# Kernel tuning notes

Hardware: AMD Instinct MI355X
Metric: run time of the kernel (lower is better)

## Reference

```python
import jax, jax.numpy as jnp
import numpy as np

B, N = 2, 1024
DIM = 1024
DQK = 128
NUM_KEYS = 256
NUM_MEM = NUM_KEYS * NUM_KEYS
TOPK = 32
RANK = 2
HEADS = 2
DV = 512
KCONV = 5
MARGIN = 0.15
AUX_W = 0.1
MEM_LR = 10.0
RMS_EPS = 1.1920929e-07  # torch.finfo(float32).eps (RMSNorm eps=None default)
LN_EPS = 1e-5


def setup_inputs() -> dict:
    key = jax.random.key(0)
    ks = jax.random.split(key, 6)
    return {
        "tokens": jax.random.normal(ks[0], (B, N, DIM), jnp.float32),
        "rms_w": jnp.ones((DIM,), jnp.float32),
        "conv_w": jax.random.normal(ks[1], (DIM, 1, KCONV), jnp.float32) * 0.1,
        "conv_b": jnp.zeros((DIM,), jnp.float32),
        "wq": jax.random.normal(ks[2], (DQK, DIM), jnp.float32) * 0.02,
        "qln_w": jnp.ones((DQK,), jnp.float32),
        "keys": jax.random.normal(ks[3], (2, RANK, NUM_KEYS, DQK), jnp.float32) * 0.01,
        "core": jax.random.normal(ks[4], (HEADS, RANK, RANK), jnp.float32) * 0.01,
        "memories": jax.random.normal(ks[5], (NUM_MEM, DV), jnp.float32) * 0.01,
    }


def _forward(tokens, rms_w, conv_w, conv_b, wq, qln_w, keys, core, memories):
    # prenorm RMSNorm
    x = tokens * jax.lax.rsqrt(jnp.mean(tokens * tokens, -1, keepdims=True) + RMS_EPS) * rms_w
    # SVD of core; rank-1 merge vectors (first left/right singular vectors)
    u, s, vh = jnp.linalg.svd(core, full_matrices=False)
    u_vec = u[..., :, 0]   # (H, R)
    t_vec = vh[..., 0, :]  # (H, R)  == v[..., :, 0]
    aux = jnp.sum(jnp.mean(jnp.square(jax.nn.relu(s[:, 1:] - MARGIN)), -1)) * AUX_W
    # causal depthwise conv (left-pad KCONV-1)
    xc = jnp.swapaxes(x, 1, 2)  # (B, D, N)
    xc = jax.lax.conv_general_dilated(
        xc, conv_w, (1,), [(KCONV - 1, 0)],
        feature_group_count=DIM, dimension_numbers=('NCH', 'OIH', 'NCH'))
    x = jnp.swapaxes(xc + conv_b[None, :, None], 1, 2)
    # queries + LayerNorm (no bias). NOTE: original applies key_ln but then uses
    # the raw self.keys in the einsum, so key normalization is a no-op; replicated.
    q = x @ wq.T
    mu = jnp.mean(q, -1, keepdims=True)
    var = jnp.mean(jnp.square(q - mu), -1, keepdims=True)
    q = (q - mu) * jax.lax.rsqrt(var + LN_EPS) * qln_w
    # product-key scores: (2, B, N, M, R)
    sc = jnp.einsum('bnd,crmd->cbnmr', q, keys)
    row_sc, col_sc = sc[0], sc[1]  # (B, N, M, R)
    m_row = jnp.einsum('bnmr,hr->hbnm', row_sc, u_vec)
    m_col = jnp.einsum('bnmr,hr->hbnm', col_sc, t_vec)
    _, top_row = jax.lax.top_k(m_row, TOPK)  # (H, B, N, K)
    _, top_col = jax.lax.top_k(m_col, TOPK)
    # candidate flat memory indices: outer sum -> (H, B, N, K*K)
    idx = (top_row * NUM_KEYS)[..., :, None] + top_col[..., None, :]
    idx = idx.reshape(HEADS, B, N, TOPK * TOPK)
    # gather per-rank scores at the top row/col keys
    rs = jnp.broadcast_to(row_sc[None], (HEADS,) + row_sc.shape)
    cs = jnp.broadcast_to(col_sc[None], (HEADS,) + col_sc.shape)
    ri = jnp.broadcast_to(top_row[..., None], top_row.shape + (RANK,))
    ci = jnp.broadcast_to(top_col[..., None], top_col.shape + (RANK,))
    f_row = jnp.take_along_axis(rs, ri, axis=3)  # (H, B, N, K, R)
    f_col = jnp.take_along_axis(cs, ci, axis=3)
    # bilinear core combine over ranks -> (H, B, N, K, K)
    scores = jnp.einsum('hbnir,hbnjs,hrs->hbnij', f_row, f_col, core)
    scores = scores.reshape(HEADS, B, N, TOPK * TOPK)
    fs, top_m = jax.lax.top_k(scores, TOPK)
    f_idx = jnp.take_along_axis(idx, top_m, axis=-1)  # (H, B, N, K)
    fs = jax.nn.sigmoid(fs)
    # gather from memory table: (H, B, N, K, DV)
    mem = memories[f_idx]
    # scale_gradient exactly as written: detach(t) - s*t + detach(s*t)  (grad = -s)
    scaled = mem * MEM_LR
    mem = jax.lax.stop_gradient(mem) - scaled + jax.lax.stop_gradient(scaled)
    agg = jnp.einsum('hbnkd,hbnk->hbnd', mem, fs)
    out = jnp.transpose(agg, (1, 2, 0, 3)).reshape(B, N, HEADS * DV)
    # combine_values_to_out is Identity (heads * dim_values == dim)
    return out, aux


def reference(tokens, rms_w, conv_w, conv_b, wq, qln_w, keys, core, memories):
    return _forward(tokens, rms_w, conv_w, conv_b, wq, qln_w, keys, core, memories)
```

## Files before the change

kernel.cpp:

```cpp
#include <hip/hip_runtime.h>
#include <math.h>


#define ROWS 2048
#define RPB 2
#define SLB (RPB + 4)
#define KSPLIT 16

__device__ inline double dsgn(double x, double y) { return (y >= 0.0) ? fabs(x) : -fabs(x); }

__device__ void dlasv2_dev(double f, double g, double h,
                           double& ssmin, double& ssmax,
                           double& snr, double& csr, double& snl, double& csl)
{
  const double EPSD = 2.2204460492503131e-16;
  double ft = f, fa = fabs(f), ht = h, ha = fabs(h);
  int pmax = 1;
  bool swp = (ha > fa);
  if (swp) { pmax = 3; double tp = ft; ft = ht; ht = tp; tp = fa; fa = ha; ha = tp; }
  double gt = g, ga = fabs(gt);
  double clt = 0.0, crt = 0.0, slt = 0.0, srt = 0.0;
  if (ga == 0.0) {
    ssmin = ha; ssmax = fa; clt = 1.0; crt = 1.0; slt = 0.0; srt = 0.0;
  } else {
    bool gasmal = true;
    if (ga > fa) {
      pmax = 2;
      if ((fa / ga) < EPSD) {
        gasmal = false;
        ssmax = ga;
        if (ha > 1.0) ssmin = fa / (ga / ha); else ssmin = (fa / ga) * ha;
        clt = 1.0; slt = ht / gt; srt = 1.0; crt = ft / gt;
      }
    }
    if (gasmal) {
      double dd = fa - ha, l;
      if (dd == fa) l = 1.0; else l = dd / fa;
      double m  = gt / ft;
      double t  = 2.0 - l;
      double mm = m * m, tt = t * t;
      double s  = sqrt(tt + mm);
      double r  = (l == 0.0) ? fabs(m) : sqrt(l * l + mm);
      double a  = 0.5 * (s + r);
      ssmin = ha / a;
      ssmax = fa * a;
      if (mm == 0.0) {
        if (l == 0.0) t = dsgn(2.0, ft) * dsgn(1.0, gt);
        else          t = gt / dsgn(dd, ft) + m / t;
      } else {
        t = (m / (s + t) + m / (r + l)) * (1.0 + a);
      }
      double ll = sqrt(t * t + 4.0);
      crt = 2.0 / ll;
      srt = t / ll;
      clt = (crt + srt * m) / a;
      slt = (ht / ft) * srt / a;
    }
  }
  if (swp) { csl = srt; snl = crt; csr = slt; snr = clt; }
  else     { csl = clt; snl = slt; csr = crt; snr = srt; }
  double tsign = 1.0;
  if (pmax == 1) tsign = dsgn(1.0, csr) * dsgn(1.0, csl) * dsgn(1.0, f);
  if (pmax == 2) tsign = dsgn(1.0, snr) * dsgn(1.0, csl) * dsgn(1.0, g);
  if (pmax == 3) tsign = dsgn(1.0, snr) * dsgn(1.0, snl) * dsgn(1.0, h);
  ssmax = dsgn(ssmax, tsign);
  ssmin = dsgn(ssmin, tsign * dsgn(1.0, f) * dsgn(1.0, h));
}

__device__ void do_svd(const float* __restrict__ core, float* __restrict__ misc,
                       float* __restrict__ aux_out)
{
  double aux = 0.0;
  for (int hh = 0; hh < 2; hh++) {
    double a = (double)core[hh * 4 + 0];
    double b = (double)core[hh * 4 + 1];
    double c = (double)core[hh * 4 + 2];
    double d = (double)core[hh * 4 + 3];
    double tau = 0.0, v2 = 0.0, d1, e, d2;
    if (c != 0.0) {
      double nrm  = sqrt(a * a + c * c);
      double beta = (a >= 0.0) ? -nrm : nrm;
      tau = (beta - a) / beta;
      v2  = c / (a - beta);
      double wsum = b + v2 * d;
      d1 = beta;
      e  = b - tau * wsum;
      d2 = d - tau * v2 * wsum;
    } else { d1 = a; e = b; d2 = d; }
    double ssmin, ssmax, snr, csr, snl, csl;
    dlasv2_dev(d1, e, d2, ssmin, ssmax, snr, csr, snl, csl);
    double t0 = csl + v2 * snl;
    double u0 = csl - tau * t0;
    double u1 = snl - tau * v2 * t0;
    double sg = (ssmax < 0.0) ? -1.0 : 1.0;
    misc[hh * 2 + 0]     = (float)u0;
    misc[hh * 2 + 1]     = (float)u1;
    misc[4 + hh * 2 + 0] = (float)(sg * csr);
    misc[4 + hh * 2 + 1] = (float)(sg * snr);
    double s2 = fabs(ssmin);
    double rl = s2 - 0.15; if (rl < 0.0) rl = 0.0;
    aux += rl * rl;
  }
  aux_out[0] = (float)(aux * 0.1);
}

__global__ __launch_bounds__(256) void conv_kernel(const float* __restrict__ tokens,
                                                   const float* __restrict__ rms_w,
                                                   const float* __restrict__ conv_w,
                                                   const float* __restrict__ conv_b,
                                                   const float* __restrict__ core,
                                                   float* __restrict__ misc,
                                                   float* __restrict__ aux_out,
                                                   float* __restrict__ x2)
{
  __shared__ float x_l[SLB][1024];
  __shared__ float red[SLB][4];
  __shared__ float inv_s[SLB];
  const int t    = threadIdx.x;
  const int row0 = blockIdx.x * RPB;
  const int n0   = row0 & 1023;
  const int c0   = t * 4;

  float sq[SLB];
  #pragma unroll
  for (int s = 0; s < SLB; s++) {
    float4 v = make_float4(0.f, 0.f, 0.f, 0.f);
    if (n0 - 4 + s >= 0)
      v = *(const float4*)(tokens + (size_t)(row0 - 4 + s) * 1024 + c0);
    *(float4*)&x_l[s][c0] = v;
    sq[s] = v.x * v.x + v.y * v.y + v.z * v.z + v.w * v.w;
  }
  #pragma unroll
  for (int off = 32; off; off >>= 1) {
    #pragma unroll
    for (int s = 0; s < SLB; s++) sq[s] += __shfl_down(sq[s], off, 64);
  }
  const int lane = t & 63, wv_id = t >> 6;
  if (lane == 0) {
    #pragma unroll
    for (int s = 0; s < SLB; s++) red[s][wv_id] = sq[s];
  }
  __syncthreads();
  if (t < SLB)
    inv_s[t] = rsqrtf((red[t][0] + red[t][1] + red[t][2] + red[t][3]) * (1.0f / 1024.0f)
                      + 1.1920929e-07f);
  __syncthreads();
  #pragma unroll
  for (int s = 0; s < SLB; s++) {
    float iv = inv_s[s];
    float4 v = *(float4*)&x_l[s][c0];
    v.x *= iv; v.y *= iv; v.z *= iv; v.w *= iv;
    *(float4*)&x_l[s][c0] = v;
  }
  float wv[20];
  const float* cw = conv_w + (size_t)c0 * 5;
  #pragma unroll
  for (int i = 0; i < 5; i++) {
    float4 u = *(const float4*)(cw + i * 4);
    wv[i * 4 + 0] = u.x; wv[i * 4 + 1] = u.y; wv[i * 4 + 2] = u.z; wv[i * 4 + 3] = u.w;
  }
  float4 rw = *(const float4*)(rms_w + c0);
  float4 cb = *(const float4*)(conv_b + c0);
  #pragma unroll
  for (int r = 0; r < RPB; r++) {
    float4 acc = make_float4(0.f, 0.f, 0.f, 0.f);
    #pragma unroll
    for (int k = 0; k < 5; k++) {
      float4 x4 = *(const float4*)&x_l[r + k][c0];
      acc.x = fmaf(x4.x, wv[0 * 5 + k], acc.x);
      acc.y = fmaf(x4.y, wv[1 * 5 + k], acc.y);
      acc.z = fmaf(x4.z, wv[2 * 5 + k], acc.z);
      acc.w = fmaf(x4.w, wv[3 * 5 + k], acc.w);
    }
    acc.x = acc.x * rw.x + cb.x;
    acc.y = acc.y * rw.y + cb.y;
    acc.z = acc.z * rw.z + cb.z;
    acc.w = acc.w * rw.w + cb.w;
    *(float4*)(x2 + (size_t)(row0 + r) * 1024 + c0) = acc;
  }
  if (blockIdx.x == 0 && t == 0) do_svd(core, misc, aux_out);
}

__global__ __launch_bounds__(256) void gemm_kernel(const float* __restrict__ A, int lda,
                                                   const float* __restrict__ Bm, int ldb,
                                                   float* __restrict__ C, int ldc,
                                                   int koffy, int coffy, int poffy)
{
  __shared__ __align__(16) float a_lds[32 * 64];
  __shared__ __align__(16) float b_lds[32 * 128];
  const int t  = threadIdx.x;
  const int rb = blockIdx.x * 64;
  const int kb = blockIdx.y * koffy;
  const int cb = blockIdx.y * coffy;
  C += (size_t)blockIdx.y * (size_t)poffy;
  const int tx = t & 31, ty = t >> 5;
  const int c0 = tx * 4, r0 = ty * 8;
  const int nkt = koffy >> 5;
  float acc[8][4];
  #pragma unroll
  for (int i = 0; i < 8; i++)
    #pragma unroll
    for (int j = 0; j < 4; j++) acc[i][j] = 0.0f;

  const int ra = t & 63,  kqa = (t >> 6) * 8;
  const int ob = t >> 1,  kqb = (t & 1) * 16;

  for (int kt = 0; kt < nkt; kt++) {
    const int k0 = kb + kt * 32;
    {
      const float* ap = A + (size_t)(rb + ra) * lda + k0 + kqa;
      float4 a0 = *(const float4*)(ap);
      float4 a1 = *(const float4*)(ap + 4);
      a_lds[(kqa + 0) * 64 + ra] = a0.x;
      a_lds[(kqa + 1) * 64 + ra] = a0.y;
      a_lds[(kqa + 2) * 64 + ra] = a0.z;
      a_lds[(kqa + 3) * 64 + ra] = a0.w;
      a_lds[(kqa + 4) * 64 + ra] = a1.x;
      a_lds[(kqa + 5) * 64 + ra] = a1.y;
      a_lds[(kqa + 6) * 64 + ra] = a1.z;
      a_lds[(kqa + 7) * 64 + ra] = a1.w;
    }
    {
      const float* bp = Bm + (size_t)(cb + ob) * ldb + k0 + kqb;
      float4 b0 = *(const float4*)(bp);
      float4 b1 = *(const float4*)(bp + 4);
      float4 b2 = *(const float4*)(bp + 8);
      float4 b3 = *(const float4*)(bp + 12);
      b_lds[(kqb +  0) * 128 + ob] = b0.x;
      b_lds[(kqb +  1) * 128 + ob] = b0.y;
      b_lds[(kqb +  2) * 128 + ob] = b0.z;
      b_lds[(kqb +  3) * 128 + ob] = b0.w;
      b_lds[(kqb +  4) * 128 + ob] = b1.x;
      b_lds[(kqb +  5) * 128 + ob] = b1.y;
      b_lds[(kqb +  6) * 128 + ob] = b1.z;
      b_lds[(kqb +  7) * 128 + ob] = b1.w;
      b_lds[(kqb +  8) * 128 + ob] = b2.x;
      b_lds[(kqb +  9) * 128 + ob] = b2.y;
      b_lds[(kqb + 10) * 128 + ob] = b2.z;
      b_lds[(kqb + 11) * 128 + ob] = b2.w;
      b_lds[(kqb + 12) * 128 + ob] = b3.x;
      b_lds[(kqb + 13) * 128 + ob] = b3.y;
      b_lds[(kqb + 14) * 128 + ob] = b3.z;
      b_lds[(kqb + 15) * 128 + ob] = b3.w;
    }
    __syncthreads();
    #pragma unroll
    for (int k = 0; k < 32; k++) {
      float4 av0 = *(const float4*)(a_lds + k * 64 + r0);
      float4 av1 = *(const float4*)(a_lds + k * 64 + r0 + 4);
      float4 bv  = *(const float4*)(b_lds + k * 128 + c0);
      float ar[8] = {av0.x, av0.y, av0.z, av0.w, av1.x, av1.y, av1.z, av1.w};
      float br[4] = {bv.x, bv.y, bv.z, bv.w};
      #pragma unroll
      for (int i = 0; i < 8; i++)
        #pragma unroll
        for (int j = 0; j < 4; j++)
          acc[i][j] = fmaf(ar[i], br[j], acc[i][j]);
    }
    __syncthreads();
  }
  #pragma unroll
  for (int i = 0; i < 8; i++) {
    float4 o4; o4.x = acc[i][0]; o4.y = acc[i][1]; o4.z = acc[i][2]; o4.w = acc[i][3];
    *(float4*)(C + (size_t)(rb + r0 + i) * ldc + cb + c0) = o4;
  }
}

__global__ __launch_bounds__(256) void gemm2ln_kernel(const float* __restrict__ qpart,
                                                      const float* __restrict__ qln_w,
                                                      const float* __restrict__ keys,
                                                      float* __restrict__ C)
{
  __shared__ __align__(16) float a_l[128 * 32];
  __shared__ __align__(16) float b_lds[32 * 128];
  const int t  = threadIdx.x;
  const int rb = blockIdx.x * 32;
  const int cb = blockIdx.y * 128;

  const int l32 = t & 31;
  const int g32 = t >> 5;
  float vs[4][4];
  #pragma unroll
  for (int j = 0; j < 4; j++) { vs[j][0]=0.f; vs[j][1]=0.f; vs[j][2]=0.f; vs[j][3]=0.f; }
  #pragma unroll
  for (int g = 0; g < KSPLIT; g++) {
    const float* pg = qpart + (size_t)g * (ROWS * 128) + (size_t)rb * 128 + l32 * 4;
    #pragma unroll
    for (int j = 0; j < 4; j++) {
      float4 v = *(const float4*)(pg + (g32 + 8 * j) * 128);
      vs[j][0] += v.x; vs[j][1] += v.y; vs[j][2] += v.z; vs[j][3] += v.w;
    }
  }
  float4 qw = *(const float4*)(qln_w + l32 * 4);
  #pragma unroll
  for (int j = 0; j < 4; j++) {
    float s1 = vs[j][0] + vs[j][1] + vs[j][2] + vs[j][3];
    #pragma unroll
    for (int off = 16; off; off >>= 1) s1 += __shfl_xor(s1, off, 32);
    float mu = s1 * (1.0f / 128.0f);
    float d0 = vs[j][0] - mu, d1 = vs[j][1] - mu, d2 = vs[j][2] - mu, d3 = vs[j][3] - mu;
    float s2 = d0 * d0 + d1 * d1 + d2 * d2 + d3 * d3;
    #pragma unroll
    for (int off = 16; off; off >>= 1) s2 += __shfl_xor(s2, off, 32);
    float rstd = rsqrtf(s2 * (1.0f / 128.0f) + 1e-5f);
    const int row = g32 + 8 * j;
    a_l[(l32 * 4 + 0) * 32 + row] = d0 * rstd * qw.x;
    a_l[(l32 * 4 + 1) * 32 + row] = d1 * rstd * qw.y;
    a_l[(l32 * 4 + 2) * 32 + row] = d2 * rstd * qw.z;
    a_l[(l32 * 4 + 3) * 32 + row] = d3 * rstd * qw.w;
  }
  __syncthreads();

  const int tx = t & 31, ty = t >> 5;
  const int c0 = tx * 4, r0 = ty * 4;
  float acc[4][4];
  #pragma unroll
  for (int i = 0; i < 4; i++)
    #pragma unroll
    for (int j = 0; j < 4; j++) acc[i][j] = 0.0f;

  const int ob = t >> 1, kqb = (t & 1) * 16;
  for (int kt = 0; kt < 4; kt++) {
    const int k0 = kt * 32;
    {
      const float* bp = keys + (size_t)(cb + ob) * 128 + k0 + kqb;
      float4 b0 = *(const float4*)(bp);
      float4 b1 = *(const float4*)(bp + 4);
      float4 b2 = *(const float4*)(bp + 8);
      float4 b3 = *(const float4*)(bp + 12);
      b_lds[(kqb +  0) * 128 + ob] = b0.x;
      b_lds[(kqb +  1) * 128 + ob] = b0.y;
      b_lds[(kqb +  2) * 128 + ob] = b0.z;
      b_lds[(kqb +  3) * 128 + ob] = b0.w;
      b_lds[(kqb +  4) * 128 + ob] = b1.x;
      b_lds[(kqb +  5) * 128 + ob] = b1.y;
      b_lds[(kqb +  6) * 128 + ob] = b1.z;
      b_lds[(kqb +  7) * 128 + ob] = b1.w;
      b_lds[(kqb +  8) * 128 + ob] = b2.x;
      b_lds[(kqb +  9) * 128 + ob] = b2.y;
      b_lds[(kqb + 10) * 128 + ob] = b2.z;
      b_lds[(kqb + 11) * 128 + ob] = b2.w;
      b_lds[(kqb + 12) * 128 + ob] = b3.x;
      b_lds[(kqb + 13) * 128 + ob] = b3.y;
      b_lds[(kqb + 14) * 128 + ob] = b3.z;
      b_lds[(kqb + 15) * 128 + ob] = b3.w;
    }
    __syncthreads();
    #pragma unroll
    for (int k = 0; k < 32; k++) {
      float4 av = *(const float4*)(a_l + (k0 + k) * 32 + r0);
      float4 bv = *(const float4*)(b_lds + k * 128 + c0);
      float ar[4] = {av.x, av.y, av.z, av.w};
      float br[4] = {bv.x, bv.y, bv.z, bv.w};
      #pragma unroll
      for (int i = 0; i < 4; i++)
        #pragma unroll
        for (int j = 0; j < 4; j++)
          acc[i][j] = fmaf(ar[i], br[j], acc[i][j]);
    }
    __syncthreads();
  }
  #pragma unroll
  for (int i = 0; i < 4; i++) {
    float4 o4; o4.x = acc[i][0]; o4.y = acc[i][1]; o4.z = acc[i][2]; o4.w = acc[i][3];
    *(float4*)(C + (size_t)(rb + r0 + i) * 1024 + cb + c0) = o4;
  }
}

__device__ inline unsigned f2ord(float f) {
  unsigned u = __float_as_uint(f);
  return (u & 0x80000000u) ? ~u : (u | 0x80000000u);
}
__device__ inline int lpc(unsigned long long m) {
  return __builtin_amdgcn_mbcnt_hi((unsigned)(m >> 32),
         __builtin_amdgcn_mbcnt_lo((unsigned)m, 0));
}

__global__ __launch_bounds__(256) void tail_kernel(const float* __restrict__ sc,
                                                   const float* __restrict__ misc,
                                                   const float* __restrict__ core,
                                                   const float* __restrict__ memories,
                                                   float* __restrict__ out)
{
  __shared__ __align__(16) float s_pl[1024];
  __shared__ int   tkbuf[4][32];
  __shared__ float mvals[4][32];
  __shared__ int   mcand[4][32];
  __shared__ int   s_idx[64];
  __shared__ float s_w[64];

  const int row = blockIdx.x;
  const int tid = threadIdx.x;
  ((float4*)s_pl)[tid] = ((const float4*)(sc + (size_t)row * 1024))[tid];
  __syncthreads();

  const int w = tid >> 6, lane = tid & 63;

  {
    const int h = w >> 1, side = w & 1;
    const float v0 = misc[side * 4 + h * 2 + 0];
    const float v1 = misc[side * 4 + h * 2 + 1];
    const float* p0 = s_pl + side * 512;
    const float* p1 = p0 + 256;
    const int mb = lane * 4;
    float4 a4 = *(const float4*)(p0 + mb);
    float4 b4 = *(const float4*)(p1 + mb);
    unsigned kk[4];
    kk[0] = f2ord(a4.x * v0 + b4.x * v1);
    kk[1] = f2ord(a4.y * v0 + b4.y * v1);
    kk[2] = f2ord(a4.z * v0 + b4.z * v1);
    kk[3] = f2ord(a4.w * v0 + b4.w * v1);
    unsigned tau = 0u;
    #pragma unroll
    for (int b = 31; b >= 0; --b) {
      unsigned cand = tau | (1u << b);
      int cnt = 0;
      #pragma unroll
      for (int i = 0; i < 4; i++) cnt += __popcll(__ballot(kk[i] >= cand));
      if (cnt >= 32) tau = cand;
    }
    unsigned long long bG[4], bE[4];
    int cntG = 0, sbG = 0, sbE = 0;
    #pragma unroll
    for (int i = 0; i < 4; i++) {
      bG[i] = __ballot(kk[i] > tau);
      bE[i] = __ballot(kk[i] == tau);
      cntG += __popcll(bG[i]);
      sbG  += lpc(bG[i]);
      sbE  += lpc(bE[i]);
    }
    const int need = 32 - cntG;
    int runG = 0, runE = 0;
    #pragma unroll
    for (int i = 0; i < 4; i++) {
      if (kk[i] > tau)       { tkbuf[w][sbG + runG] = mb + i; runG++; }
      else if (kk[i] == tau) {
        int r = sbE + runE;
        if (r < need) tkbuf[w][cntG + r] = mb + i;
        runE++;
      }
    }
  }
  __syncthreads();

  {
    const int h = w >> 1, half = w & 1;
    const float c00 = core[h * 4 + 0], c01 = core[h * 4 + 1];
    const float c10 = core[h * 4 + 2], c11 = core[h * 4 + 3];
    const int i_glob = half * 16 + (lane >> 2);
    const int ri = tkbuf[h * 2 + 0][i_glob];
    const float fr0 = s_pl[ri], fr1 = s_pl[256 + ri];
    const float a0 = fr0 * c00 + fr1 * c10;
    const float a1 = fr0 * c01 + fr1 * c11;
    const int j0 = (lane & 3) * 8;
    float sv[8];
    unsigned kk[8];
    #pragma unroll
    for (int t2 = 0; t2 < 8; t2++) {
      int cj = tkbuf[h * 2 + 1][j0 + t2];
      sv[t2] = a0 * s_pl[512 + cj] + a1 * s_pl[768 + cj];
      kk[t2] = f2ord(sv[t2]);
    }
    unsigned tau = 0u;
    #pragma unroll
    for (int b = 31; b >= 0; --b) {
      unsigned cand = tau | (1u << b);
      int cnt = 0;
      #pragma unroll
      for (int i = 0; i < 8; i++) cnt += __popcll(__ballot(kk[i] >= cand));
      if (cnt >= 32) tau = cand;
    }
    unsigned long long bG[8], bE[8];
    int cntG = 0, sbG = 0, sbE = 0;
    #pragma unroll
    for (int i = 0; i < 8; i++) {
      bG[i] = __ballot(kk[i] > tau);
      bE[i] = __ballot(kk[i] == tau);
      cntG += __popcll(bG[i]);
      sbG  += lpc(bG[i]);
      sbE  += lpc(bE[i]);
    }
    const int need = 32 - cntG;
    int runG = 0, runE = 0;
    #pragma unroll
    for (int i = 0; i < 8; i++) {
      int c = i_glob * 32 + j0 + i;
      if (kk[i] > tau) {
        mvals[w][sbG + runG] = sv[i]; mcand[w][sbG + runG] = c; runG++;
      } else if (kk[i] == tau) {
        int r = sbE + runE;
        if (r < need) { mvals[w][cntG + r] = sv[i]; mcand[w][cntG + r] = c; }
        runE++;
      }
    }
  }
  __syncthreads();

  if (w < 2) {
    const int h = w;
    const int half2 = lane >> 5, k = lane & 31;
    const float v = mvals[h * 2 + half2][k];
    const int   c = mcand[h * 2 + half2][k];
    int cnt = 0;
    #pragma unroll 8
    for (int j = 0; j < 64; j++) {
      float u = mvals[h * 2 + (j >> 5)][j & 31];
      int  uc = mcand[h * 2 + (j >> 5)][j & 31];
      cnt += (u > v || (u == v && uc < c)) ? 1 : 0;
    }
    if (cnt < 32) {
      int ii = c >> 5, jj = c & 31;
      s_idx[h * 32 + cnt] = tkbuf[h * 2][ii] * 256 + tkbuf[h * 2 + 1][jj];
      s_w[h * 32 + cnt]   = 1.0f / (1.0f + expf(-v));
    }
  }
  __syncthreads();

  const int h2 = tid >> 7;
  const int d4 = tid & 127;
  const int base = h2 * 32;
  const float* mb = memories + d4 * 4;
  float ax = 0.f, ay = 0.f, az = 0.f, aw = 0.f;
  float4 va[8], vb[8];
  float  wa[8], wb[8];
  #pragma unroll
  for (int i = 0; i < 8; i++) {
    int mi = s_idx[base + i]; wa[i] = s_w[base + i];
    va[i] = *(const float4*)(mb + (size_t)mi * 512);
  }
  #pragma unroll
  for (int i = 0; i < 8; i++) {
    int mi = s_idx[base + 8 + i]; wb[i] = s_w[base + 8 + i];
    vb[i] = *(const float4*)(mb + (size_t)mi * 512);
  }
  #pragma unroll
  for (int i = 0; i < 8; i++) {
    ax = fmaf(wa[i], va[i].x, ax); ay = fmaf(wa[i], va[i].y, ay);
    az = fmaf(wa[i], va[i].z, az); aw = fmaf(wa[i], va[i].w, aw);
  }
  #pragma unroll
  for (int i = 0; i < 8; i++) {
    int mi = s_idx[base + 16 + i]; wa[i] = s_w[base + 16 + i];
    va[i] = *(const float4*)(mb + (size_t)mi * 512);
  }
  #pragma unroll
  for (int i = 0; i < 8; i++) {
    ax = fmaf(wb[i], vb[i].x, ax); ay = fmaf(wb[i], vb[i].y, ay);
    az = fmaf(wb[i], vb[i].z, az); aw = fmaf(wb[i], vb[i].w, aw);
  }
  #pragma unroll
  for (int i = 0; i < 8; i++) {
    int mi = s_idx[base + 24 + i]; wb[i] = s_w[base + 24 + i];
    vb[i] = *(const float4*)(mb + (size_t)mi * 512);
  }
  #pragma unroll
  for (int i = 0; i < 8; i++) {
    ax = fmaf(wa[i], va[i].x, ax); ay = fmaf(wa[i], va[i].y, ay);
    az = fmaf(wa[i], va[i].z, az); aw = fmaf(wa[i], va[i].w, aw);
  }
  #pragma unroll
  for (int i = 0; i < 8; i++) {
    ax = fmaf(wb[i], vb[i].x, ax); ay = fmaf(wb[i], vb[i].y, ay);
    az = fmaf(wb[i], vb[i].z, az); aw = fmaf(wb[i], vb[i].w, aw);
  }
  float4 o4; o4.x = ax; o4.y = ay; o4.z = az; o4.w = aw;
  ((float4*)out)[(size_t)row * 256 + tid] = o4;
}

extern "C" void kernel_launch(void* const* d_in, const int* in_sizes, int n_in,
                              void* d_out, int out_size, void* d_ws, size_t ws_size,
                              hipStream_t stream) {
  const float* tokens = (const float*)d_in[0];
  const float* rms_w  = (const float*)d_in[1];
  const float* conv_w = (const float*)d_in[2];
  const float* conv_b = (const float*)d_in[3];
  const float* wq     = (const float*)d_in[4];
  const float* qln_w  = (const float*)d_in[5];
  const float* keys   = (const float*)d_in[6];
  const float* core   = (const float*)d_in[7];
  const float* mems   = (const float*)d_in[8];
  float* out = (float*)d_out;
  float* ws  = (float*)d_ws;

  float* misc   = ws;
  float* x2     = ws + 4096;
  float* qpart  = x2 + 2097152;
  float* sc     = x2;

  conv_kernel  <<<ROWS / RPB, 256, 0, stream>>>(tokens, rms_w, conv_w, conv_b,
                                                core, misc, out + 2097152, x2);
  gemm_kernel  <<<dim3(32, KSPLIT), 256, 0, stream>>>(x2, 1024, wq, 1024,
                                                      qpart, 128, 1024 / KSPLIT, 0,
                                                      ROWS * 128);
  gemm2ln_kernel<<<dim3(64, 8), 256, 0, stream>>>(qpart, qln_w, keys, sc);
  tail_kernel  <<<ROWS, 256, 0, stream>>>(sc, misc, core, mems, out);
}
```

Before: 275.9 us.

## Fuse causal depthwise conv into query GEMM A-tile load, keep only RMS stats

Replaces the conv kernel, which wrote the full convolved activation to workspace, with a small kernel that only computes per-row RMS scale factors plus the SVD. The depthwise conv is now computed on the fly inside the query GEMM while it builds the A tile in shared memory, using a 68-row halo of tokens. This removes an 8 MB write and re-read of the intermediate activation. In exchange the GEMM does redundant conv work and halo loads, the split-K factor drops from 16 to 8, and each block now runs a longer 128-wide K loop with extra syncs.

```diff
diff --git a/kernel.cpp b/kernel.cpp
--- a/kernel.cpp
+++ b/kernel.cpp
@@ -3,9 +3,7 @@
 
 
 #define ROWS 2048
-#define RPB 2
-#define SLB (RPB + 4)
-#define KSPLIT 16
+#define KSPLIT 8
 
 __device__ inline double dsgn(double x, double y) { return (y >= 0.0) ? fabs(x) : -fabs(x); }
 
@@ -104,151 +102,119 @@
   aux_out[0] = (float)(aux * 0.1);
 }
 
-__global__ __launch_bounds__(256) void conv_kernel(const float* __restrict__ tokens,
-                                                   const float* __restrict__ rms_w,
-                                                   const float* __restrict__ conv_w,
-                                                   const float* __restrict__ conv_b,
-                                                   const float* __restrict__ core,
-                                                   float* __restrict__ misc,
-                                                   float* __restrict__ aux_out,
-                                                   float* __restrict__ x2)
+__global__ __launch_bounds__(256) void rms_kernel(const float* __restrict__ tokens,
+                                                  const float* __restrict__ core,
+                                                  float* __restrict__ inv_sg,
+                                                  float* __restrict__ misc,
+                                                  float* __restrict__ aux_out)
 {
-  __shared__ float x_l[SLB][1024];
-  __shared__ float red[SLB][4];
-  __shared__ float inv_s[SLB];
+  __shared__ float red[8][4];
   const int t    = threadIdx.x;
-  const int row0 = blockIdx.x * RPB;
-  const int n0   = row0 & 1023;
+  const int row0 = blockIdx.x * 8;
   const int c0   = t * 4;
-
-  float sq[SLB];
-  #pragma unroll
-  for (int s = 0; s < SLB; s++) {
-    float4 v = make_float4(0.f, 0.f, 0.f, 0.f);
-    if (n0 - 4 + s >= 0)
-      v = *(const float4*)(tokens + (size_t)(row0 - 4 + s) * 1024 + c0);
-    *(float4*)&x_l[s][c0] = v;
+  float sq[8];
+  #pragma unroll
+  for (int s = 0; s < 8; s++) {
+    float4 v = *(const float4*)(tokens + (size_t)(row0 + s) * 1024 + c0);
     sq[s] = v.x * v.x + v.y * v.y + v.z * v.z + v.w * v.w;
   }
   #pragma unroll
   for (int off = 32; off; off >>= 1) {
     #pragma unroll
-    for (int s = 0; s < SLB; s++) sq[s] += __shfl_down(sq[s], off, 64);
-  }
-  const int lane = t & 63, wv_id = t >> 6;
+    for (int s = 0; s < 8; s++) sq[s] += __shfl_down(sq[s], off, 64);
+  }
+  const int lane = t & 63, w = t >> 6;
   if (lane == 0) {
     #pragma unroll
-    for (int s = 0; s < SLB; s++) red[s][wv_id] = sq[s];
+    for (int s = 0; s < 8; s++) red[s][w] = sq[s];
   }
   __syncthreads();
-  if (t < SLB)
-    inv_s[t] = rsqrtf((red[t][0] + red[t][1] + red[t][2] + red[t][3]) * (1.0f / 1024.0f)
-                      + 1.1920929e-07f);
-  __syncthreads();
-  #pragma unroll
-  for (int s = 0; s < SLB; s++) {
-    float iv = inv_s[s];
-    float4 v = *(float4*)&x_l[s][c0];
-    v.x *= iv; v.y *= iv; v.z *= iv; v.w *= iv;
-    *(float4*)&x_l[s][c0] = v;
-  }
-  float wv[20];
-  const float* cw = conv_w + (size_t)c0 * 5;
-  #pragma unroll
-  for (int i = 0; i < 5; i++) {
-    float4 u = *(const float4*)(cw + i * 4);
-    wv[i * 4 + 0] = u.x; wv[i * 4 + 1] = u.y; wv[i * 4 + 2] = u.z; wv[i * 4 + 3] = u.w;
-  }
-  float4 rw = *(const float4*)(rms_w + c0);
-  float4 cb = *(const float4*)(conv_b + c0);
-  #pragma unroll
-  for (int r = 0; r < RPB; r++) {
-    float4 acc = make_float4(0.f, 0.f, 0.f, 0.f);
-    #pragma unroll
-    for (int k = 0; k < 5; k++) {
-      float4 x4 = *(const float4*)&x_l[r + k][c0];
-      acc.x = fmaf(x4.x, wv[0 * 5 + k], acc.x);
-      acc.y = fmaf(x4.y, wv[1 * 5 + k], acc.y);
-      acc.z = fmaf(x4.z, wv[2 * 5 + k], acc.z);
-      acc.w = fmaf(x4.w, wv[3 * 5 + k], acc.w);
-    }
-    acc.x = acc.x * rw.x + cb.x;
-    acc.y = acc.y * rw.y + cb.y;
-    acc.z = acc.z * rw.z + cb.z;
-    acc.w = acc.w * rw.w + cb.w;
-    *(float4*)(x2 + (size_t)(row0 + r) * 1024 + c0) = acc;
-  }
+  if (t < 8)
+    inv_sg[row0 + t] = rsqrtf((red[t][0] + red[t][1] + red[t][2] + red[t][3])
+                              * (1.0f / 1024.0f) + 1.1920929e-07f);
   if (blockIdx.x == 0 && t == 0) do_svd(core, misc, aux_out);
 }
 
-__global__ __launch_bounds__(256) void gemm_kernel(const float* __restrict__ A, int lda,
-                                                   const float* __restrict__ Bm, int ldb,
-                                                   float* __restrict__ C, int ldc,
-                                                   int koffy, int coffy, int poffy)
+__global__ __launch_bounds__(256) void convgemm1_kernel(
+    const float* __restrict__ tokens, const float* __restrict__ inv_sg,
+    const float* __restrict__ rms_w,  const float* __restrict__ conv_w,
+    const float* __restrict__ conv_b, const float* __restrict__ wq,
+    float* __restrict__ qpart)
 {
+  __shared__ float xh[68 * 33];
   __shared__ __align__(16) float a_lds[32 * 64];
   __shared__ __align__(16) float b_lds[32 * 128];
+  __shared__ float inv_l[68];
   const int t  = threadIdx.x;
   const int rb = blockIdx.x * 64;
-  const int kb = blockIdx.y * koffy;
-  const int cb = blockIdx.y * coffy;
-  C += (size_t)blockIdx.y * (size_t)poffy;
+  const int kb = blockIdx.y * 128;
+  const int n0 = rb & 1023;
+
+  if (t < 68) inv_l[t] = (n0 - 4 + t >= 0) ? inv_sg[rb - 4 + t] : 0.0f;
+
   const int tx = t & 31, ty = t >> 5;
-  const int c0 = tx * 4, r0 = ty * 8;
-  const int nkt = koffy >> 5;
+  const int c0g = tx * 4, r0 = ty * 8;
   float acc[8][4];
   #pragma unroll
   for (int i = 0; i < 8; i++)
     #pragma unroll
     for (int j = 0; j < 4; j++) acc[i][j] = 0.0f;
 
-  const int ra = t & 63,  kqa = (t >> 6) * 8;
-  const int ob = t >> 1,  kqb = (t & 1) * 16;
-
-  for (int kt = 0; kt < nkt; kt++) {
+  const int ob = t >> 1, kqb = (t & 1) * 16;
+  const int cr = t & 63;
+  const int ch = (t >> 6) * 8;
+
+  for (int kt = 0; kt < 4; kt++) {
     const int k0 = kb + kt * 32;
+    __syncthreads();
+    #pragma unroll
+    for (int it = 0; it < 3; it++) {
+      int idx  = it * 256 + t;
+      int srow = idx >> 3, f4 = (idx & 7) * 4;
+      if (srow < 68) {
+        float4 v = make_float4(0.f, 0.f, 0.f, 0.f);
+        if (n0 - 4 + srow >= 0)
+          v = *(const float4*)(tokens + (size_t)(rb - 4 + srow) * 1024 + k0 + f4);
+        float iv = inv_l[srow];
+        xh[srow * 33 + f4 + 0] = v.x * iv;
+        xh[srow * 33 + f4 + 1] = v.y * iv;
+        xh[srow * 33 + f4 + 2] = v.z * iv;
+        xh[srow * 33 + f4 + 3] = v.w * iv;
+      }
+    }
     {
-      const float* ap = A + (size_t)(rb + ra) * lda + k0 + kqa;
-      float4 a0 = *(const float4*)(ap);
-      float4 a1 = *(const float4*)(ap + 4);
-      a_lds[(kqa + 0) * 64 + ra] = a0.x;
-      a_lds[(kqa + 1) * 64 + ra] = a0.y;
-      a_lds[(kqa + 2) * 64 + ra] = a0.z;
-      a_lds[(kqa + 3) * 64 + ra] = a0.w;
-      a_lds[(kqa + 4) * 64 + ra] = a1.x;
-      a_lds[(kqa + 5) * 64 + ra] = a1.y;
-      a_lds[(kqa + 6) * 64 + ra] = a1.z;
-      a_lds[(kqa + 7) * 64 + ra] = a1.w;
-    }
-    {
-      const float* bp = Bm + (size_t)(cb + ob) * ldb + k0 + kqb;
+      const float* bp = wq + (size_t)ob * 1024 + k0 + kqb;
       float4 b0 = *(const float4*)(bp);
       float4 b1 = *(const float4*)(bp + 4);
       float4 b2 = *(const float4*)(bp + 8);
       float4 b3 = *(const float4*)(bp + 12);
-      b_lds[(kqb +  0) * 128 + ob] = b0.x;
-      b_lds[(kqb +  1) * 128 + ob] = b0.y;
-      b_lds[(kqb +  2) * 128 + ob] = b0.z;
-      b_lds[(kqb +  3) * 128 + ob] = b0.w;
-      b_lds[(kqb +  4) * 128 + ob] = b1.x;
-      b_lds[(kqb +  5) * 128 + ob] = b1.y;
-      b_lds[(kqb +  6) * 128 + ob] = b1.z;
-      b_lds[(kqb +  7) * 128 + ob] = b1.w;
-      b_lds[(kqb +  8) * 128 + ob] = b2.x;
-      b_lds[(kqb +  9) * 128 + ob] = b2.y;
-      b_lds[(kqb + 10) * 128 + ob] = b2.z;
-      b_lds[(kqb + 11) * 128 + ob] = b2.w;
-      b_lds[(kqb + 12) * 128 + ob] = b3.x;
-      b_lds[(kqb + 13) * 128 + ob] = b3.y;
-      b_lds[(kqb + 14) * 128 + ob] = b3.z;
-      b_lds[(kqb + 15) * 128 + ob] = b3.w;
+      b_lds[(kqb +  0) * 128 + ob] = b0.x;  b_lds[(kqb +  1) * 128 + ob] = b0.y;
+      b_lds[(kqb +  2) * 128 + ob] = b0.z;  b_lds[(kqb +  3) * 128 + ob] = b0.w;
+      b_lds[(kqb +  4) * 128 + ob] = b1.x;  b_lds[(kqb +  5) * 128 + ob] = b1.y;
+      b_lds[(kqb +  6) * 128 + ob] = b1.z;  b_lds[(kqb +  7) * 128 + ob] = b1.w;
+      b_lds[(kqb +  8) * 128 + ob] = b2.x;  b_lds[(kqb +  9) * 128 + ob] = b2.y;
+      b_lds[(kqb + 10) * 128 + ob] = b2.z;  b_lds[(kqb + 11) * 128 + ob] = b2.w;
+      b_lds[(kqb + 12) * 128 + ob] = b3.x;  b_lds[(kqb + 13) * 128 + ob] = b3.y;
+      b_lds[(kqb + 14) * 128 + ob] = b3.z;  b_lds[(kqb + 15) * 128 + ob] = b3.w;
+    }
+    __syncthreads();
+    #pragma unroll
+    for (int i = 0; i < 8; i++) {
+      const int c = ch + i;
+      const float* cw = conv_w + (size_t)(k0 + c) * 5;
+      float a = xh[(cr + 0) * 33 + c] * cw[0]
+              + xh[(cr + 1) * 33 + c] * cw[1]
+              + xh[(cr + 2) * 33 + c] * cw[2]
+              + xh[(cr + 3) * 33 + c] * cw[3]
+              + xh[(cr + 4) * 33 + c] * cw[4];
+      a_lds[c * 64 + cr] = a * rms_w[k0 + c] + conv_b[k0 + c];
     }
     __syncthreads();
     #pragma unroll
     for (int k = 0; k < 32; k++) {
       float4 av0 = *(const float4*)(a_lds + k * 64 + r0);
       float4 av1 = *(const float4*)(a_lds + k * 64 + r0 + 4);
-      float4 bv  = *(const float4*)(b_lds + k * 128 + c0);
+      float4 bv  = *(const float4*)(b_lds + k * 128 + c0g);
       float ar[8] = {av0.x, av0.y, av0.z, av0.w, av1.x, av1.y, av1.z, av1.w};
       float br[4] = {bv.x, bv.y, bv.z, bv.w};
       #pragma unroll
@@ -257,12 +223,12 @@
         for (int j = 0; j < 4; j++)
           acc[i][j] = fmaf(ar[i], br[j], acc[i][j]);
     }
-    __syncthreads();
-  }
+  }
+  float* C = qpart + (size_t)blockIdx.y * (ROWS * 128);
   #pragma unroll
   for (int i = 0; i < 8; i++) {
     float4 o4; o4.x = acc[i][0]; o4.y = acc[i][1]; o4.z = acc[i][2]; o4.w = acc[i][3];
-    *(float4*)(C + (size_t)(rb + r0 + i) * ldc + cb + c0) = o4;
+    *(float4*)(C + (size_t)(rb + r0 + i) * 128 + c0g) = o4;
   }
 }
 
@@ -328,22 +294,14 @@
       float4 b1 = *(const float4*)(bp + 4);
       float4 b2 = *(const float4*)(bp + 8);
       float4 b3 = *(const float4*)(bp + 12);
-      b_lds[(kqb +  0) * 128 + ob] = b0.x;
-      b_lds[(kqb +  1) * 128 + ob] = b0.y;
-      b_lds[(kqb +  2) * 128 + ob] = b0.z;
-      b_lds[(kqb +  3) * 128 + ob] = b0.w;
-      b_lds[(kqb +  4) * 128 + ob] = b1.x;
-      b_lds[(kqb +  5) * 128 + ob] = b1.y;
-      b_lds[(kqb +  6) * 128 + ob] = b1.z;
-      b_lds[(kqb +  7) * 128 + ob] = b1.w;
-      b_lds[(kqb +  8) * 128 + ob] = b2.x;
-      b_lds[(kqb +  9) * 128 + ob] = b2.y;
-      b_lds[(kqb + 10) * 128 + ob] = b2.z;
-      b_lds[(kqb + 11) * 128 + ob] = b2.w;
-      b_lds[(kqb + 12) * 128 + ob] = b3.x;
-      b_lds[(kqb + 13) * 128 + ob] = b3.y;
-      b_lds[(kqb + 14) * 128 + ob] = b3.z;
-      b_lds[(kqb + 15) * 128 + ob] = b3.w;
+      b_lds[(kqb +  0) * 128 + ob] = b0.x;  b_lds[(kqb +  1) * 128 + ob] = b0.y;
+      b_lds[(kqb +  2) * 128 + ob] = b0.z;  b_lds[(kqb +  3) * 128 + ob] = b0.w;
+      b_lds[(kqb +  4) * 128 + ob] = b1.x;  b_lds[(kqb +  5) * 128 + ob] = b1.y;
+      b_lds[(kqb +  6) * 128 + ob] = b1.z;  b_lds[(kqb +  7) * 128 + ob] = b1.w;
+      b_lds[(kqb +  8) * 128 + ob] = b2.x;  b_lds[(kqb +  9) * 128 + ob] = b2.y;
+      b_lds[(kqb + 10) * 128 + ob] = b2.z;  b_lds[(kqb + 11) * 128 + ob] = b2.w;
+      b_lds[(kqb + 12) * 128 + ob] = b3.x;  b_lds[(kqb + 13) * 128 + ob] = b3.y;
+      b_lds[(kqb + 14) * 128 + ob] = b3.z;  b_lds[(kqb + 15) * 128 + ob] = b3.w;
     }
     __syncthreads();
     #pragma unroll
@@ -582,16 +540,15 @@
   float* out = (float*)d_out;
   float* ws  = (float*)d_ws;
 
-  float* misc   = ws;
-  float* x2     = ws + 4096;
-  float* qpart  = x2 + 2097152;
-  float* sc     = x2;
-
-  conv_kernel  <<<ROWS / RPB, 256, 0, stream>>>(tokens, rms_w, conv_w, conv_b,
-                                                core, misc, out + 2097152, x2);
-  gemm_kernel  <<<dim3(32, KSPLIT), 256, 0, stream>>>(x2, 1024, wq, 1024,
-                                                      qpart, 128, 1024 / KSPLIT, 0,
-                                                      ROWS * 128);
-  gemm2ln_kernel<<<dim3(64, 8), 256, 0, stream>>>(qpart, qln_w, keys, sc);
-  tail_kernel  <<<ROWS, 256, 0, stream>>>(sc, misc, core, mems, out);
-}
+  float* misc  = ws;
+  float* invs  = ws + 1024;
+  float* qpart = ws + 4096;
+  float* sc    = qpart + 2097152;
+
+  rms_kernel     <<<ROWS / 8, 256, 0, stream>>>(tokens, core, invs, misc,
+                                                out + 2097152);
+  convgemm1_kernel<<<dim3(32, KSPLIT), 256, 0, stream>>>(tokens, invs, rms_w,
+                                                         conv_w, conv_b, wq, qpart);
+  gemm2ln_kernel <<<dim3(64, 8), 256, 0, stream>>>(qpart, qln_w, keys, sc);
+  tail_kernel    <<<ROWS, 256, 0, stream>>>(sc, misc, core, mems, out);
+}
```

After: 280.0 us. About the same (+1.5%).
